# Optimization experiments

Hardware: AMD Instinct MI355X
Metric: run time of the kernel (lower is better)

Reference implementation:

```python
import jax, jax.numpy as jnp
import numpy as np

B, L, H = 16, 512, 1024
K_START, K_END = 5, 5
LN_EPS = 1e-12
NEG = 1e30


def _layer_norm(x, gamma, beta):
    mu = jnp.mean(x, axis=-1, keepdims=True)
    var = jnp.mean(jnp.square(x - mu), axis=-1, keepdims=True)
    return (x - mu) * jax.lax.rsqrt(var + LN_EPS) * gamma + beta


def setup_inputs() -> dict:
    key = jax.random.key(0)
    ks = jax.random.split(key, 10)
    s = 0.02
    sequence_data = jax.random.normal(ks[0], (B, L, H), jnp.float32)
    class_index = jax.random.randint(ks[1], (B,), 0, L, dtype=jnp.int32)
    paragraph_mask = (jax.random.uniform(ks[2], (B, L)) > 0.1).astype(jnp.float32)
    paragraph_mask = paragraph_mask.at[:, 0].set(1.0)  # guarantee >=1 valid position per row
    return {
        'sequence_data': sequence_data,
        'class_index': class_index,
        'paragraph_mask': paragraph_mask,
        'W_start': jax.random.normal(ks[3], (H, 1), jnp.float32) * s,
        'b_start': jnp.zeros((1,), jnp.float32),
        'W_end_in': jax.random.normal(ks[4], (2 * H, H), jnp.float32) * s,
        'b_end_in': jnp.zeros((H,), jnp.float32),
        'ln_gamma': jnp.ones((H,), jnp.float32),
        'ln_beta': jnp.zeros((H,), jnp.float32),
        'W_end_out': jax.random.normal(ks[5], (H, 1), jnp.float32) * s,
        'b_end_out': jnp.zeros((1,), jnp.float32),
        'W_ans_in': jax.random.normal(ks[6], (2 * H, H), jnp.float32) * s,
        'b_ans_in': jnp.zeros((H,), jnp.float32),
        'W_ans_out': jax.random.normal(ks[7], (H, 1), jnp.float32) * s,
    }


def reference(sequence_data, class_index, paragraph_mask,
              W_start, b_start, W_end_in, b_end_in, ln_gamma, ln_beta,
              W_end_out, b_end_out, W_ans_in, b_ans_in, W_ans_out):
    mask = paragraph_mask  # [b, l] float, 1 = valid

    # ---- start logits ----
    start_logits = jnp.einsum('blh,ho->bl', sequence_data, W_start) + b_start[0]  # [b,l]
    masked_start_logits = start_logits * mask - NEG * (1.0 - mask)
    start_predictions = jax.nn.log_softmax(masked_start_logits, axis=-1)

    # ---- beam search over start positions (inference branch) ----
    start_top_predictions, start_top_index = jax.lax.top_k(start_predictions, K_START)  # [b,k]
    # one-hot einsum gather 'blh,bkl->bkh' expressed as direct indexing
    start_features = jnp.take_along_axis(sequence_data, start_top_index[:, :, None], axis=1)  # [b,k,h]

    # end_logits inner dense on concat([tiled seq, tiled start_features]) along h:
    # split the [2h, h] kernel and broadcast-add instead of materializing the tiled concat.
    W1, W2 = W_end_in[:H], W_end_in[H:]
    inner = jnp.tanh(
        jnp.einsum('blh,hd->bld', sequence_data, W1)[:, :, None, :]
        + jnp.einsum('bkh,hd->bkd', start_features, W2)[:, None, :, :]
        + b_end_in
    )  # [b,l,k,h]
    inner = _layer_norm(inner, ln_gamma, ln_beta)
    end_logits = jnp.einsum('blkh,ho->blk', inner, W_end_out) + b_end_out[0]  # [b,l,k]
    end_logits = jnp.transpose(end_logits, (0, 2, 1))  # [b,k,l]

    mask_k = mask[:, None, :]  # [b,1,l]
    masked_end_logits = end_logits * mask_k - NEG * (1.0 - mask_k)
    end_predictions = jax.nn.log_softmax(masked_end_logits, axis=-1)

    end_top_predictions, _end_top_index = jax.lax.top_k(end_predictions, K_END)  # [b,k,k2]
    end_top_predictions = end_top_predictions.reshape(-1, K_START * K_END)

    # ---- answer (class) logits ----
    class_feature = sequence_data[jnp.arange(sequence_data.shape[0]), class_index]  # [b,h]
    start_p = jax.nn.softmax(masked_start_logits, axis=-1)
    start_feature = jnp.einsum('blh,bl->bh', sequence_data, start_p)
    answer_feature = jnp.concatenate([start_feature, class_feature], axis=-1)  # [b,2h]
    answer_feature = jnp.tanh(answer_feature @ W_ans_in + b_ans_in)  # dropout is identity at inference
    class_logits = (answer_feature @ W_ans_out)[:, 0]  # [b]

    return (start_predictions, end_predictions, masked_start_logits, masked_end_logits,
            start_top_predictions, end_top_predictions, class_logits)
```

## Files before the change

### kernel.cpp

```cpp
#include <hip/hip_runtime.h>
#include <math.h>

#define HD   1024
#define LSEQ 512
#define NB   16
#define KTOP 5
#define NEGV 1e30f

typedef __bf16 bf16x8 __attribute__((ext_vector_type(8)));
typedef float  f32x4  __attribute__((ext_vector_type(4)));

__device__ inline unsigned short f2bf(float f) {
  unsigned u = __float_as_uint(f);
  unsigned r = (u + 0x7FFFu + ((u >> 16) & 1u)) >> 16;
  return (unsigned short)r;
}
__device__ inline float bf2f(unsigned short u) {
  return __uint_as_float(((unsigned)u) << 16);
}

__device__ inline float fast_tanh(float x) {
  float e = __expf(-2.f * fabsf(x));
  float v = (1.f - e) / (1.f + e);
  return copysignf(v, x);
}

__device__ inline float tanh_scaled(float xs) {
  float e = __builtin_amdgcn_exp2f(xs);
  float r = __builtin_amdgcn_rcpf(1.f + e);
  return fmaf(-2.f, r, 1.f);
}

#define GLDS(g, l) __builtin_amdgcn_global_load_lds(                      \
    (const __attribute__((address_space(1))) unsigned int*)(g),          \
    (__attribute__((address_space(3))) unsigned int*)(l), 16, 0, 0)


__device__ __forceinline__ void sm_body(int row, const float* __restrict__ xin,
                                        float* __restrict__ lsm_out,
                                        float* __restrict__ top_out,
                                        float* __restrict__ p_out,
                                        int* __restrict__ idx_out) {
  __shared__ float redf[4];
  __shared__ int redi[4];
  __shared__ float bc_m, bc_s;
  __shared__ int bc_i;
  int t = threadIdx.x, lane = t & 63, wid = t >> 6;
  const float* x = xin + (size_t)row * LSEQ;
  float x0 = x[t], x1 = x[t + 256];

  float m = fmaxf(x0, x1);
#pragma unroll
  for (int off = 32; off; off >>= 1) m = fmaxf(m, __shfl_xor(m, off));
  if (lane == 0) redf[wid] = m;
  __syncthreads();
  if (t == 0) bc_m = fmaxf(fmaxf(redf[0], redf[1]), fmaxf(redf[2], redf[3]));
  __syncthreads();
  m = bc_m;

  float e0 = expf(x0 - m), e1 = expf(x1 - m);
  float s = e0 + e1;
#pragma unroll
  for (int off = 32; off; off >>= 1) s += __shfl_xor(s, off);
  if (lane == 0) redf[wid] = s;
  __syncthreads();
  if (t == 0) bc_s = redf[0] + redf[1] + redf[2] + redf[3];
  __syncthreads();
  s = bc_s;
  float ls = logf(s);

  lsm_out[(size_t)row * LSEQ + t] = x0 - m - ls;
  lsm_out[(size_t)row * LSEQ + t + 256] = x1 - m - ls;
  if (p_out) {
    float inv = 1.f / s;
    p_out[(size_t)row * LSEQ + t] = e0 * inv;
    p_out[(size_t)row * LSEQ + t + 256] = e1 * inv;
  }

  bool a0 = true, a1 = true;
  for (int it = 0; it < KTOP; ++it) {
    float v0 = a0 ? x0 : -INFINITY;
    float v1 = a1 ? x1 : -INFINITY;
    float bv = v0; int bi = t;
    if (v1 > bv) { bv = v1; bi = t + 256; }
#pragma unroll
    for (int off = 32; off; off >>= 1) {
      float ov = __shfl_xor(bv, off);
      int oi = __shfl_xor(bi, off);
      if (ov > bv || (ov == bv && oi < bi)) { bv = ov; bi = oi; }
    }
    __syncthreads();
    if (lane == 0) { redf[wid] = bv; redi[wid] = bi; }
    __syncthreads();
    if (t == 0) {
      float wv = redf[0]; int wi = redi[0];
      for (int w = 1; w < 4; ++w)
        if (redf[w] > wv || (redf[w] == wv && redi[w] < wi)) { wv = redf[w]; wi = redi[w]; }
      top_out[row * KTOP + it] = wv - m - ls;
      if (idx_out) idx_out[row * KTOP + it] = wi;
      bc_i = wi;
    }
    __syncthreads();
    int wi = bc_i;
    if (wi == t) a0 = false;
    if (wi == t + 256) a1 = false;
  }
}

__device__ __forceinline__ void gemm_body(int R0, int C0,
                                          const unsigned short* __restrict__ Abf,
                                          const unsigned short* __restrict__ Bt,
                                          unsigned short* __restrict__ X1) {
  __shared__ unsigned short SH[16384];
  unsigned short* As = SH;
  unsigned short* Bs = SH + 8192;
  int t = threadIdx.x;
  int w = t >> 6, lane = t & 63, ln = lane & 15, hi = lane >> 4;
  int wr = w >> 1, wc = w & 1;

  f32x4 acc[4][4] = {};

#define STAGE(kc)                                                             \
  do {                                                                        \
    _Pragma("unroll")                                                         \
    for (int p_ = 0; p_ < 4; ++p_) {                                          \
      int rr_ = p_ * 32 + (t >> 3);                                           \
      int cc_ = (t & 7) ^ (rr_ & 7);                                          \
      GLDS(Abf + (size_t)(R0 + rr_) * HD + (kc) + cc_ * 8,                    \
           As + p_ * 2048 + w * 512);                                         \
      GLDS(Bt + (size_t)(C0 + rr_) * HD + (kc) + cc_ * 8,                     \
           Bs + p_ * 2048 + w * 512);                                         \
    }                                                                         \
  } while (0)

  for (int it = 0; it < 16; ++it) {
    if (it) __syncthreads();
    STAGE(it * 64);
    asm volatile("s_waitcnt vmcnt(0)" ::: "memory");
    __builtin_amdgcn_s_barrier();
#pragma unroll
    for (int ks = 0; ks < 2; ++ks) {
      bf16x8 av[4], bv[4];
#pragma unroll
      for (int m = 0; m < 4; ++m) {
        int r = wr * 64 + m * 16 + ln;
        av[m] = *(const bf16x8*)(const void*)&As[r * 64 + (((ks * 4 + hi) ^ (r & 7)) * 8)];
      }
#pragma unroll
      for (int n = 0; n < 4; ++n) {
        int r = wc * 64 + n * 16 + ln;
        bv[n] = *(const bf16x8*)(const void*)&Bs[r * 64 + (((ks * 4 + hi) ^ (r & 7)) * 8)];
      }
#pragma unroll
      for (int m = 0; m < 4; ++m)
#pragma unroll
        for (int n = 0; n < 4; ++n)
          acc[m][n] = __builtin_amdgcn_mfma_f32_16x16x32_bf16(av[m], bv[n], acc[m][n], 0, 0, 0);
    }
  }
#undef STAGE

#pragma unroll
  for (int m = 0; m < 4; ++m)
#pragma unroll
    for (int j = 0; j < 4; ++j) {
      int row = R0 + wr * 64 + m * 16 + hi * 4 + j;
#pragma unroll
      for (int n = 0; n < 4; ++n) {
        int col = C0 + wc * 64 + n * 16 + ln;
        X1[(size_t)row * HD + col] = f2bf(acc[m][n][j]);
      }
    }
}

__device__ __forceinline__ void x2gemm_body(int cid,
                                            const unsigned short* __restrict__ seqb,
                                            const unsigned short* __restrict__ w2t,
                                            const int* __restrict__ idx,
                                            const float* __restrict__ bei,
                                            float* __restrict__ x2p) {
  __shared__ unsigned short SH2[16384];
  unsigned short* As = SH2;
  unsigned short* Bs = SH2 + 8192;
  int t = threadIdx.x;
  int w = t >> 6, lane = t & 63, ln = lane & 15, hi = lane >> 4;
  int wr = w >> 1, wc = w & 1;
  int C0 = cid * 128;

  size_t abase[4];
#pragma unroll
  for (int p_ = 0; p_ < 4; ++p_) {
    int rr = p_ * 32 + (t >> 3);
    int bk = rr < 80 ? rr : 0;
    int l = idx[bk];
    abase[p_] = ((size_t)((bk / KTOP) * LSEQ + l)) * HD;
  }

  f32x4 acc[4][4] = {};

#define STAGE2(kc)                                                            \
  do {                                                                        \
    _Pragma("unroll")                                                         \
    for (int p_ = 0; p_ < 4; ++p_) {                                          \
      int rr_ = p_ * 32 + (t >> 3);                                           \
      int cc_ = (t & 7) ^ (rr_ & 7);                                          \
      GLDS(seqb + abase[p_] + (kc) + cc_ * 8,                                 \
           As + p_ * 2048 + w * 512);                                         \
      GLDS(w2t + (size_t)(C0 + rr_) * HD + (kc) + cc_ * 8,                    \
           Bs + p_ * 2048 + w * 512);                                         \
    }                                                                         \
  } while (0)

  for (int it = 0; it < 16; ++it) {
    if (it) __syncthreads();
    STAGE2(it * 64);
    asm volatile("s_waitcnt vmcnt(0)" ::: "memory");
    __builtin_amdgcn_s_barrier();
#pragma unroll
    for (int ks = 0; ks < 2; ++ks) {
      bf16x8 av[4], bv[4];
#pragma unroll
      for (int m = 0; m < 4; ++m) {
        int r = wr * 64 + m * 16 + ln;
        av[m] = *(const bf16x8*)(const void*)&As[r * 64 + (((ks * 4 + hi) ^ (r & 7)) * 8)];
      }
#pragma unroll
      for (int n = 0; n < 4; ++n) {
        int r = wc * 64 + n * 16 + ln;
        bv[n] = *(const bf16x8*)(const void*)&Bs[r * 64 + (((ks * 4 + hi) ^ (r & 7)) * 8)];
      }
#pragma unroll
      for (int m = 0; m < 4; ++m)
#pragma unroll
        for (int n = 0; n < 4; ++n)
          acc[m][n] = __builtin_amdgcn_mfma_f32_16x16x32_bf16(av[m], bv[n], acc[m][n], 0, 0, 0);
    }
  }
#undef STAGE2

#pragma unroll
  for (int m = 0; m < 4; ++m)
#pragma unroll
    for (int j = 0; j < 4; ++j) {
      int row = wr * 64 + m * 16 + hi * 4 + j;
      if (row < 80) {
#pragma unroll
        for (int n = 0; n < 4; ++n) {
          int col = C0 + wc * 64 + n * 16 + ln;
          x2p[(size_t)row * HD + col] = acc[m][n][j] + bei[col];
        }
      }
    }
}

__device__ __forceinline__ void ansin_body(int q, const float* __restrict__ seq,
                                           const float* __restrict__ p_ws,
                                           const int* __restrict__ cls,
                                           float* __restrict__ pa,
                                           float* __restrict__ cf) {
  __shared__ float ps[16];
  int b = q >> 5, s = q & 31, t = threadIdx.x;
  if (t < 16) ps[t] = p_ws[b * LSEQ + s * 16 + t];
  __syncthreads();
  const float* sb = seq + (size_t)(b * LSEQ + s * 16) * HD;
  float4 acc = make_float4(0.f, 0.f, 0.f, 0.f);
#pragma unroll
  for (int r = 0; r < 16; ++r) {
    float4 v = *(const float4*)(sb + (size_t)r * HD + 4 * t);
    float p = ps[r];
    acc.x = fmaf(p, v.x, acc.x);
    acc.y = fmaf(p, v.y, acc.y);
    acc.z = fmaf(p, v.z, acc.z);
    acc.w = fmaf(p, v.w, acc.w);
  }
  *(float4*)(pa + ((size_t)b * 32 + s) * HD + 4 * t) = acc;
  if (s == 0) {
    int ci = cls[b];
    *(float4*)(cf + (size_t)b * HD + 4 * t) =
        *(const float4*)(seq + (size_t)(b * LSEQ + ci) * HD + 4 * t);
  }
}

__device__ __forceinline__ void endrow_body(int bx, const unsigned short* __restrict__ X1,
                                            const float* __restrict__ x2p,
                                            const float* __restrict__ gw_ws,
                                            const float* __restrict__ sgb_ws,
                                            const float* __restrict__ mask,
                                            float* __restrict__ mel) {
  __shared__ float x2s[KTOP * HD];
  const float A = 2.885390081777927f;
  int t = threadIdx.x, wave = t >> 6, lane = t & 63;
  int row = bx * 4 + wave;
  int b = row >> 9, l = row & 511;

  {
    const float4* src = (const float4*)(x2p + (size_t)b * KTOP * HD);
    float4* dst = (float4*)x2s;
    for (int i = t; i < KTOP * HD / 4; i += 256) {
      float4 v = src[i];
      dst[i] = make_float4(v.x * A, v.y * A, v.z * A, v.w * A);
    }
  }

  float xs[16], gwr[16];
  const unsigned short* xrow = X1 + (size_t)row * HD + lane * 4;
#pragma unroll
  for (int q = 0; q < 4; ++q) {
    ushort4 u = *(const ushort4*)(xrow + q * 256);
    xs[4 * q + 0] = bf2f(u.x) * A;
    xs[4 * q + 1] = bf2f(u.y) * A;
    xs[4 * q + 2] = bf2f(u.z) * A;
    xs[4 * q + 3] = bf2f(u.w) * A;
    float4 g = *(const float4*)(gw_ws + q * 256 + lane * 4);
    gwr[4 * q + 0] = g.x; gwr[4 * q + 1] = g.y;
    gwr[4 * q + 2] = g.z; gwr[4 * q + 3] = g.w;
  }
  float mv = mask[row];
  float sG = sgb_ws[0], sBW = sgb_ws[1];
  __syncthreads();

#pragma unroll
  for (int k = 0; k < KTOP; ++k) {
    float sv = 0.f, s2 = 0.f, sg = 0.f;
#pragma unroll
    for (int q = 0; q < 4; ++q) {
      float4 xq = *(const float4*)&x2s[k * HD + q * 256 + lane * 4];
      float v0 = tanh_scaled(xs[4 * q + 0] + xq.x);
      float v1 = tanh_scaled(xs[4 * q + 1] + xq.y);
      float v2 = tanh_scaled(xs[4 * q + 2] + xq.z);
      float v3 = tanh_scaled(xs[4 * q + 3] + xq.w);
      sv += v0 + v1 + v2 + v3;
      s2 = fmaf(v0, v0, s2); s2 = fmaf(v1, v1, s2);
      s2 = fmaf(v2, v2, s2); s2 = fmaf(v3, v3, s2);
      sg = fmaf(v0, gwr[4 * q + 0], sg); sg = fmaf(v1, gwr[4 * q + 1], sg);
      sg = fmaf(v2, gwr[4 * q + 2], sg); sg = fmaf(v3, gwr[4 * q + 3], sg);
    }
#pragma unroll
    for (int off = 32; off; off >>= 1) {
      sv += __shfl_xor(sv, off);
      s2 += __shfl_xor(s2, off);
      sg += __shfl_xor(sg, off);
    }
    if (lane == 0) {
      float mu = sv * (1.f / (float)HD);
      float var = s2 * (1.f / (float)HD) - mu * mu;
      float rr = rsqrtf(var + 1e-12f);
      float logit = rr * (sg - mu * sG) + sBW;
      mel[((size_t)b * KTOP + k) * LSEQ + l] = logit * mv - NEGV * (1.f - mv);
    }
  }
}

__device__ __forceinline__ void ansmid_body(int q, const float* __restrict__ pa,
                                            const float* __restrict__ cf,
                                            const float* __restrict__ Wai,
                                            float* __restrict__ pans) {
  __shared__ float a_s[128];
  int b = q >> 4, c = q & 15, t = threadIdx.x;
  if (t < 128) {
    int i = c * 128 + t;
    float av;
    if (i < HD) {
      av = 0.f;
#pragma unroll
      for (int s = 0; s < 32; ++s) av += pa[((size_t)b * 32 + s) * HD + i];
    } else {
      av = cf[(size_t)b * HD + (i - HD)];
    }
    a_s[t] = av;
  }
  __syncthreads();
  float4 acc = make_float4(0.f, 0.f, 0.f, 0.f);
#pragma unroll 8
  for (int r = 0; r < 128; ++r) {
    float4 wv = *(const float4*)(Wai + (size_t)(c * 128 + r) * HD + 4 * t);
    float a = a_s[r];
    acc.x = fmaf(a, wv.x, acc.x);
    acc.y = fmaf(a, wv.y, acc.y);
    acc.z = fmaf(a, wv.z, acc.z);
    acc.w = fmaf(a, wv.w, acc.w);
  }
  *(float4*)(pans + ((size_t)b * 16 + c) * HD + 4 * t) = acc;
}

__device__ __forceinline__ void ansfinal_body(int b, const float* __restrict__ pans,
                                              const float* __restrict__ bai,
                                              const float* __restrict__ Wao,
                                              float* __restrict__ out6) {
  __shared__ float red[4];
  int t = threadIdx.x, lane = t & 63, wid = t >> 6;
  float4 a = *(const float4*)(bai + 4 * t);
#pragma unroll
  for (int c = 0; c < 16; ++c) {
    float4 p = *(const float4*)(pans + ((size_t)b * 16 + c) * HD + 4 * t);
    a.x += p.x; a.y += p.y; a.z += p.z; a.w += p.w;
  }
  float4 wo = *(const float4*)(Wao + 4 * t);
  float part = fast_tanh(a.x) * wo.x + fast_tanh(a.y) * wo.y +
               fast_tanh(a.z) * wo.z + fast_tanh(a.w) * wo.w;
#pragma unroll
  for (int off = 32; off; off >>= 1) part += __shfl_xor(part, off);
  if (lane == 0) red[wid] = part;
  __syncthreads();
  if (t == 0) out6[b] = red[0] + red[1] + red[2] + red[3];
}


__global__ void k_prep(const float* __restrict__ seq,
                       unsigned short* __restrict__ seqb,
                       const float* __restrict__ Wst,
                       const float* __restrict__ bst,
                       const float* __restrict__ mask,
                       float* __restrict__ msl,
                       const float* __restrict__ Wei,
                       unsigned short* __restrict__ w1t,
                       unsigned short* __restrict__ w2t,
                       const float* __restrict__ gam,
                       const float* __restrict__ bet,
                       const float* __restrict__ Weo,
                       const float* __restrict__ beo,
                       float* __restrict__ gw_ws,
                       float* __restrict__ sgb_ws) {
  __shared__ unsigned short tile[32][33];
  __shared__ float redp[4][2];
  int bx = blockIdx.x;
  if (bx < 2048) {
    int wave = threadIdx.x >> 6, lane = threadIdx.x & 63;
    int row = bx * 4 + wave;
    const float4* s4 = (const float4*)(seq + (size_t)row * HD);
    const float4* w4 = (const float4*)Wst;
    ushort4* o4 = (ushort4*)(seqb + (size_t)row * HD);
    float acc = 0.f;
#pragma unroll
    for (int m = 0; m < 4; ++m) {
      int i = lane + 64 * m;
      float4 a = s4[i], w = w4[i];
      acc += a.x * w.x + a.y * w.y + a.z * w.z + a.w * w.w;
      ushort4 o;
      o.x = f2bf(a.x); o.y = f2bf(a.y); o.z = f2bf(a.z); o.w = f2bf(a.w);
      o4[i] = o;
    }
#pragma unroll
    for (int off = 32; off; off >>= 1) acc += __shfl_xor(acc, off);
    if (lane == 0) {
      float logit = acc + bst[0];
      float mv = mask[row];
      msl[row] = logit * mv - NEGV * (1.f - mv);
    }
  } else if (bx < 4096) {
    int tb = bx - 2048;
    const float* Wsrc = Wei + (tb >= 1024 ? (size_t)HD * HD : 0);
    unsigned short* Wdst = (tb >= 1024) ? w2t : w1t;
    int tb2 = tb & 1023;
    int h0 = (tb2 & 31) * 32, d0 = (tb2 >> 5) * 32;
    int tx = threadIdx.x & 31, ty = threadIdx.x >> 5;
#pragma unroll
    for (int i = 0; i < 4; ++i)
      tile[ty + 8 * i][tx] = f2bf(Wsrc[(size_t)(h0 + ty + 8 * i) * HD + d0 + tx]);
    __syncthreads();
#pragma unroll
    for (int i = 0; i < 4; ++i)
      Wdst[(size_t)(d0 + ty + 8 * i) * HD + h0 + tx] = tile[tx][ty + 8 * i];
  } else {
    int t = threadIdx.x, wave = t >> 6, lane = t & 63;
    float4 g = ((const float4*)gam)[t];
    float4 w = ((const float4*)Weo)[t];
    float4 bv = ((const float4*)bet)[t];
    float4 gwv = make_float4(g.x * w.x, g.y * w.y, g.z * w.z, g.w * w.w);
    ((float4*)gw_ws)[t] = gwv;
    float pg = gwv.x + gwv.y + gwv.z + gwv.w;
    float pb = bv.x * w.x + bv.y * w.y + bv.z * w.z + bv.w * w.w;
#pragma unroll
    for (int off = 32; off; off >>= 1) {
      pg += __shfl_xor(pg, off);
      pb += __shfl_xor(pb, off);
    }
    if (lane == 0) { redp[wave][0] = pg; redp[wave][1] = pb; }
    __syncthreads();
    if (t == 0) {
      sgb_ws[0] = redp[0][0] + redp[1][0] + redp[2][0] + redp[3][0];
      sgb_ws[1] = redp[0][1] + redp[1][1] + redp[2][1] + redp[3][1] + beo[0];
    }
  }
}

__global__ void k_softmax_topk(const float* __restrict__ xin,
                               float* __restrict__ lsm_out,
                               float* __restrict__ top_out,
                               float* __restrict__ p_out,
                               int* __restrict__ idx_out) {
  sm_body(blockIdx.x, xin, lsm_out, top_out, p_out, idx_out);
}

__launch_bounds__(256, 4)
__global__ void k_gsm(const unsigned short* __restrict__ Abf,
                      const unsigned short* __restrict__ Bt,
                      unsigned short* __restrict__ X1,
                      const float* __restrict__ msl,
                      float* __restrict__ lsm_out,
                      float* __restrict__ top_out,
                      float* __restrict__ p_out,
                      int* __restrict__ idx_out) {
  int id = blockIdx.x;
  if (id < 16) {
    sm_body(id, msl, lsm_out, top_out, p_out, idx_out);
  } else {
    int gid = id - 16;
    gemm_body((gid & 63) * 128, (gid >> 6) * 128, Abf, Bt, X1);
  }
}

__launch_bounds__(256, 4)
__global__ void k_x2a(const unsigned short* __restrict__ seqb,
                      const unsigned short* __restrict__ w2t,
                      const int* __restrict__ idx,
                      const float* __restrict__ bei,
                      float* __restrict__ x2p,
                      const float* __restrict__ seq,
                      const float* __restrict__ p_ws,
                      const int* __restrict__ cls,
                      float* __restrict__ pa,
                      float* __restrict__ cf) {
  int id = blockIdx.x;
  if (id < 8) x2gemm_body(id, seqb, w2t, idx, bei, x2p);
  else ansin_body(id - 8, seq, p_ws, cls, pa, cf);
}

__global__ void k_end2(const unsigned short* __restrict__ X1,
                       const float* __restrict__ x2p,
                       const float* __restrict__ gw_ws,
                       const float* __restrict__ sgb_ws,
                       const float* __restrict__ mask,
                       float* __restrict__ mel,
                       const float* __restrict__ pa,
                       const float* __restrict__ cf,
                       const float* __restrict__ Wai,
                       float* __restrict__ pans) {
  int bx = blockIdx.x;
  if (bx < 2048) endrow_body(bx, X1, x2p, gw_ws, sgb_ws, mask, mel);
  else ansmid_body(bx - 2048, pa, cf, Wai, pans);
}

__global__ void k_fin(const float* __restrict__ mel,
                      float* __restrict__ lsm_out,
                      float* __restrict__ top_out,
                      const float* __restrict__ pans,
                      const float* __restrict__ bai,
                      const float* __restrict__ Wao,
                      float* __restrict__ out6) {
  int bx = blockIdx.x;
  if (bx < NB * KTOP) sm_body(bx, mel, lsm_out, top_out, nullptr, nullptr);
  else ansfinal_body(bx - NB * KTOP, pans, bai, Wao, out6);
}

__global__ void k_x2init(const float* __restrict__ bei, float* __restrict__ x2p) {
  ((float4*)(x2p + (size_t)blockIdx.x * HD))[threadIdx.x] = ((const float4*)bei)[threadIdx.x];
}

__global__ void k_x2f(const float* __restrict__ seq, const int* __restrict__ idx,
                      const float* __restrict__ Wei, float* __restrict__ x2p) {
  __shared__ float srow[128];
  int q = blockIdx.x;
  int bk = q >> 3, s = q & 7, t = threadIdx.x;
  int b = bk / KTOP;
  int l = idx[bk];
  if (t < 128) srow[t] = seq[((size_t)(b * LSEQ + l)) * HD + s * 128 + t];
  __syncthreads();
  const float* W2 = Wei + (size_t)HD * HD + (size_t)s * 128 * HD;
  float4 acc = make_float4(0.f, 0.f, 0.f, 0.f);
#pragma unroll 8
  for (int h = 0; h < 128; ++h) {
    float4 wv = *(const float4*)(W2 + (size_t)h * HD + 4 * t);
    float sv = srow[h];
    acc.x = fmaf(sv, wv.x, acc.x);
    acc.y = fmaf(sv, wv.y, acc.y);
    acc.z = fmaf(sv, wv.z, acc.z);
    acc.w = fmaf(sv, wv.w, acc.w);
  }
  float* dst = x2p + (size_t)bk * HD + 4 * t;
  atomicAdd(dst + 0, acc.x);
  atomicAdd(dst + 1, acc.y);
  atomicAdd(dst + 2, acc.z);
  atomicAdd(dst + 3, acc.w);
}

__global__ void k_ansin_f(const float* __restrict__ seq, const float* __restrict__ p_ws,
                          const int* __restrict__ cls, float* __restrict__ pa,
                          float* __restrict__ cf) {
  ansin_body(blockIdx.x, seq, p_ws, cls, pa, cf);
}
__global__ void k_ansmid_f(const float* __restrict__ pa, const float* __restrict__ cf,
                           const float* __restrict__ Wai, float* __restrict__ pans) {
  ansmid_body(blockIdx.x, pa, cf, Wai, pans);
}

__launch_bounds__(256, 2)
__global__ void k_gemm_end_at(const unsigned short* __restrict__ Abf,
                              const unsigned short* __restrict__ Bt,
                              const float* __restrict__ x2p,
                              const float* __restrict__ gamma,
                              const float* __restrict__ Wout,
                              float* __restrict__ outp) {
  __shared__ unsigned short As[2][128 * 64];
  __shared__ unsigned short Bs[2][128 * 64];
  int t = threadIdx.x;
  int w = t >> 6, lane = t & 63, ln = lane & 15, hi = lane >> 4;
  int wr = w >> 1, wc = w & 1;
  int R0 = blockIdx.x * 128, C0 = blockIdx.y * 128;
  int b = R0 >> 9;
  f32x4 acc[4][4] = {};
#define STAGE(buf, kc)                                                        \
  do {                                                                        \
    _Pragma("unroll")                                                         \
    for (int p_ = 0; p_ < 4; ++p_) {                                          \
      int rr_ = p_ * 32 + (t >> 3);                                           \
      int cc_ = (t & 7) ^ (rr_ & 7);                                          \
      GLDS(Abf + (size_t)(R0 + rr_) * HD + (kc) + cc_ * 8,                    \
           &As[buf][p_ * 2048 + w * 512]);                                    \
      GLDS(Bt + (size_t)(C0 + rr_) * HD + (kc) + cc_ * 8,                     \
           &Bs[buf][p_ * 2048 + w * 512]);                                    \
    }                                                                         \
  } while (0)
  STAGE(0, 0);
  for (int it = 0; it < 16; ++it) {
    int cur = it & 1;
    if (it < 15) {
      STAGE(cur ^ 1, (it + 1) * 64);
      asm volatile("s_waitcnt vmcnt(8)" ::: "memory");
    } else {
      asm volatile("s_waitcnt vmcnt(0)" ::: "memory");
    }
    __builtin_amdgcn_s_barrier();
    __builtin_amdgcn_sched_barrier(0);
#pragma unroll
    for (int ks = 0; ks < 2; ++ks) {
      bf16x8 av[4], bv[4];
#pragma unroll
      for (int m = 0; m < 4; ++m) {
        int r = wr * 64 + m * 16 + ln;
        av[m] = *(const bf16x8*)(const void*)&As[cur][r * 64 + (((ks * 4 + hi) ^ (r & 7)) * 8)];
      }
#pragma unroll
      for (int n = 0; n < 4; ++n) {
        int r = wc * 64 + n * 16 + ln;
        bv[n] = *(const bf16x8*)(const void*)&Bs[cur][r * 64 + (((ks * 4 + hi) ^ (r & 7)) * 8)];
      }
#pragma unroll
      for (int m = 0; m < 4; ++m)
#pragma unroll
        for (int n = 0; n < 4; ++n)
          acc[m][n] = __builtin_amdgcn_mfma_f32_16x16x32_bf16(av[m], bv[n], acc[m][n], 0, 0, 0);
    }
    __builtin_amdgcn_sched_barrier(0);
    __builtin_amdgcn_s_barrier();
  }
#undef STAGE
  float gsv[4];
  float x2v[4][KTOP];
#pragma unroll
  for (int n = 0; n < 4; ++n) {
    int c = C0 + wc * 64 + n * 16 + ln;
    gsv[n] = gamma[c] * Wout[c];
#pragma unroll
    for (int k = 0; k < KTOP; ++k) x2v[n][k] = x2p[((size_t)b * KTOP + k) * HD + c];
  }
#pragma unroll
  for (int m = 0; m < 4; ++m)
#pragma unroll
    for (int j = 0; j < 4; ++j) {
      int row = R0 + wr * 64 + m * 16 + hi * 4 + j;
#pragma unroll
      for (int k = 0; k < KTOP; ++k) {
        float sv = 0.f, s2 = 0.f, sg = 0.f;
#pragma unroll
        for (int n = 0; n < 4; ++n) {
          float v = fast_tanh(acc[m][n][j] + x2v[n][k]);
          sv += v; s2 += v * v; sg += v * gsv[n];
        }
#pragma unroll
        for (int off = 8; off; off >>= 1) {
          sv += __shfl_xor(sv, off);
          s2 += __shfl_xor(s2, off);
          sg += __shfl_xor(sg, off);
        }
        if (ln == 0) {
          float* p = outp + ((size_t)row * KTOP + k) * 3;
          atomicAdd(p, sv);
          atomicAdd(p + 1, s2);
          atomicAdd(p + 2, sg);
        }
      }
    }
}

__global__ void k_end_final(const float* __restrict__ sums,
                            const float* __restrict__ gamma,
                            const float* __restrict__ beta,
                            const float* __restrict__ Wout,
                            const float* __restrict__ beo,
                            const float* __restrict__ mask,
                            float* __restrict__ mel) {
  int bk = blockIdx.x, b = bk / KTOP, k = bk % KTOP;
  int t = threadIdx.x, lane = t & 63, wid = t >> 6;
  __shared__ float red[4][2];
  float pg = 0.f, pb = 0.f;
  for (int i = t; i < HD; i += 256) {
    float wv = Wout[i];
    pg += gamma[i] * wv;
    pb += beta[i] * wv;
  }
#pragma unroll
  for (int off = 32; off; off >>= 1) {
    pg += __shfl_xor(pg, off);
    pb += __shfl_xor(pb, off);
  }
  if (lane == 0) { red[wid][0] = pg; red[wid][1] = pb; }
  __syncthreads();
  float sG = red[0][0] + red[1][0] + red[2][0] + red[3][0];
  float sBW = red[0][1] + red[1][1] + red[2][1] + red[3][1] + beo[0];
  for (int l = t; l < LSEQ; l += 256) {
    int row = b * LSEQ + l;
    const float* s = sums + ((size_t)row * KTOP + k) * 3;
    float sv = s[0], s2 = s[1], sg = s[2];
    float mu = sv * (1.f / (float)HD);
    float var = s2 * (1.f / (float)HD) - mu * mu;
    float rr = rsqrtf(var + 1e-12f);
    float logit = rr * (sg - mu * sG) + sBW;
    float mv = mask[row];
    mel[((size_t)b * KTOP + k) * LSEQ + l] = logit * mv - NEGV * (1.f - mv);
  }
}

extern "C" void kernel_launch(void* const* d_in, const int* in_sizes, int n_in,
                              void* d_out, int out_size, void* d_ws, size_t ws_size,
                              hipStream_t stream) {
  (void)in_sizes; (void)n_in; (void)out_size;
  const float* seq = (const float*)d_in[0];
  const int*   cls = (const int*)d_in[1];
  const float* mask = (const float*)d_in[2];
  const float* Wst = (const float*)d_in[3];
  const float* bst = (const float*)d_in[4];
  const float* Wei = (const float*)d_in[5];
  const float* bei = (const float*)d_in[6];
  const float* gam = (const float*)d_in[7];
  const float* bet = (const float*)d_in[8];
  const float* Weo = (const float*)d_in[9];
  const float* beo = (const float*)d_in[10];
  const float* Wai = (const float*)d_in[11];
  const float* bai = (const float*)d_in[12];
  const float* Wao = (const float*)d_in[13];

  float* out = (float*)d_out;
  float* out0 = out;
  float* out1 = out0 + 8192;
  float* out2 = out1 + 40960;
  float* out3 = out2 + 8192;
  float* out4 = out3 + 40960;
  float* out5 = out4 + 80;
  float* out6 = out5 + 400;

  char* p = (char*)d_ws;
  unsigned short* seqb = (unsigned short*)p;  p += (size_t)8192 * 1024 * 2;
  unsigned short* w1t  = (unsigned short*)p;  p += (size_t)1024 * 1024 * 2;
  unsigned short* w2t  = (unsigned short*)p;  p += (size_t)1024 * 1024 * 2;
  float* p_ws   = (float*)p;                  p += 8192 * 4;
  int*   idx_ws = (int*)p;                    p += 128 * 4;
  float* x2p    = (float*)p;                  p += (size_t)80 * 1024 * 4;
  float* gw_ws  = (float*)p;                  p += 1024 * 4;
  float* sgb_ws = (float*)p;                  p += 4 * 4;
  float* pa     = (float*)p;                  p += (size_t)16 * 32 * 1024 * 4;
  float* cf     = (float*)p;                  p += (size_t)16 * 1024 * 4;
  float* pans   = (float*)p;                  p += (size_t)16 * 16 * 1024 * 4;
  unsigned short* x1 = (unsigned short*)p;
  float* sums = (float*)p;
  size_t base = (size_t)(p - (char*)d_ws);
  size_t need_big = base + (size_t)8192 * 1024 * 2;
  size_t need_small = base + (size_t)8192 * KTOP * 3 * 4;

  k_prep<<<4097, 256, 0, stream>>>(seq, seqb, Wst, bst, mask, out2, Wei, w1t, w2t,
                                   gam, bet, Weo, beo, gw_ws, sgb_ws);

  if (ws_size >= need_big) {
    k_gsm<<<528, 256, 0, stream>>>(seqb, w1t, x1, out2, out0, out4, p_ws, idx_ws);
    k_x2a<<<520, 256, 0, stream>>>(seqb, w2t, idx_ws, bei, x2p,
                                   seq, p_ws, cls, pa, cf);
    k_end2<<<2304, 256, 0, stream>>>(x1, x2p, gw_ws, sgb_ws, mask, out3,
                                     pa, cf, Wai, pans);
  } else if (ws_size >= need_small) {
    k_softmax_topk<<<NB, 256, 0, stream>>>(out2, out0, out4, p_ws, idx_ws);
    k_x2init<<<80, 256, 0, stream>>>(bei, x2p);
    k_x2f<<<640, 256, 0, stream>>>(seq, idx_ws, Wei, x2p);
    hipMemsetAsync(sums, 0, (size_t)8192 * KTOP * 3 * sizeof(float), stream);
    k_gemm_end_at<<<dim3(64, 8), 256, 0, stream>>>(seqb, w1t, x2p, gam, Weo, sums);
    k_end_final<<<NB * KTOP, 256, 0, stream>>>(sums, gam, bet, Weo, beo, mask, out3);
    k_ansin_f<<<512, 256, 0, stream>>>(seq, p_ws, cls, pa, cf);
    k_ansmid_f<<<256, 256, 0, stream>>>(pa, cf, Wai, pans);
  }

  k_fin<<<96, 256, 0, stream>>>(out3, out1, out5, pans, bai, Wao, out6);
}
```

Measured before the change: 87.92 us.

## Rebalance fused kernels: move answer pooling into GEMM launch, ansmid into x2 launch

The start-softmax-weighted pooling now recomputes the softmax probabilities per block and reads bf16 sequence data. This lets it run in the first fused launch, interleaved with the big GEMM tiles. The answer-mid matvec moves into the x2 GEMM launch, leaving the end-row kernel to do only its own work. Shared memory is shared across the fused bodies through explicit pointers. The aim is to shorten the critical path by overlapping the small answer-branch work with the heavy GEMM phases. The cost is redundant softmax work per block and bf16 precision for the pooled feature.

```diff
diff --git a/kernel.cpp b/kernel.cpp
--- a/kernel.cpp
+++ b/kernel.cpp
@@ -36,15 +36,15 @@
     (__attribute__((address_space(3))) unsigned int*)(l), 16, 0, 0)
 
 
-__device__ __forceinline__ void sm_body(int row, const float* __restrict__ xin,
+__device__ __forceinline__ void sm_body(float* sc, int row, const float* __restrict__ xin,
                                         float* __restrict__ lsm_out,
                                         float* __restrict__ top_out,
                                         float* __restrict__ p_out,
                                         int* __restrict__ idx_out) {
-  __shared__ float redf[4];
-  __shared__ int redi[4];
-  __shared__ float bc_m, bc_s;
-  __shared__ int bc_i;
+  float* redf = sc;
+  int* redi = (int*)(sc + 4);
+  float* bc = sc + 8;
+  int* bci = (int*)(sc + 10);
   int t = threadIdx.x, lane = t & 63, wid = t >> 6;
   const float* x = xin + (size_t)row * LSEQ;
   float x0 = x[t], x1 = x[t + 256];
@@ -54,9 +54,9 @@
   for (int off = 32; off; off >>= 1) m = fmaxf(m, __shfl_xor(m, off));
   if (lane == 0) redf[wid] = m;
   __syncthreads();
-  if (t == 0) bc_m = fmaxf(fmaxf(redf[0], redf[1]), fmaxf(redf[2], redf[3]));
-  __syncthreads();
-  m = bc_m;
+  if (t == 0) bc[0] = fmaxf(fmaxf(redf[0], redf[1]), fmaxf(redf[2], redf[3]));
+  __syncthreads();
+  m = bc[0];
 
   float e0 = expf(x0 - m), e1 = expf(x1 - m);
   float s = e0 + e1;
@@ -64,9 +64,9 @@
   for (int off = 32; off; off >>= 1) s += __shfl_xor(s, off);
   if (lane == 0) redf[wid] = s;
   __syncthreads();
-  if (t == 0) bc_s = redf[0] + redf[1] + redf[2] + redf[3];
-  __syncthreads();
-  s = bc_s;
+  if (t == 0) bc[1] = redf[0] + redf[1] + redf[2] + redf[3];
+  __syncthreads();
+  s = bc[1];
   float ls = logf(s);
 
   lsm_out[(size_t)row * LSEQ + t] = x0 - m - ls;
@@ -98,20 +98,19 @@
         if (redf[w] > wv || (redf[w] == wv && redi[w] < wi)) { wv = redf[w]; wi = redi[w]; }
       top_out[row * KTOP + it] = wv - m - ls;
       if (idx_out) idx_out[row * KTOP + it] = wi;
-      bc_i = wi;
+      bci[0] = wi;
     }
     __syncthreads();
-    int wi = bc_i;
+    int wi = bci[0];
     if (wi == t) a0 = false;
     if (wi == t + 256) a1 = false;
   }
 }
 
-__device__ __forceinline__ void gemm_body(int R0, int C0,
+__device__ __forceinline__ void gemm_body(unsigned short* SH, int R0, int C0,
                                           const unsigned short* __restrict__ Abf,
                                           const unsigned short* __restrict__ Bt,
                                           unsigned short* __restrict__ X1) {
-  __shared__ unsigned short SH[16384];
   unsigned short* As = SH;
   unsigned short* Bs = SH + 8192;
   int t = threadIdx.x;
@@ -173,13 +172,12 @@
     }
 }
 
-__device__ __forceinline__ void x2gemm_body(int cid,
+__device__ __forceinline__ void x2gemm_body(unsigned short* SH2, int cid,
                                             const unsigned short* __restrict__ seqb,
                                             const unsigned short* __restrict__ w2t,
                                             const int* __restrict__ idx,
                                             const float* __restrict__ bei,
                                             float* __restrict__ x2p) {
-  __shared__ unsigned short SH2[16384];
   unsigned short* As = SH2;
   unsigned short* Bs = SH2 + 8192;
   int t = threadIdx.x;
@@ -253,6 +251,59 @@
     }
 }
 
+__device__ __forceinline__ void ansin_ms_body(float* sc, int q,
+                                              const unsigned short* __restrict__ seqb,
+                                              const float* __restrict__ seq,
+                                              const float* __restrict__ msl,
+                                              const int* __restrict__ cls,
+                                              float* __restrict__ pa,
+                                              float* __restrict__ cf) {
+  float* ared = sc;
+  float* abc = sc + 4;
+  float* ps = sc + 6;
+  int b = q >> 5, sl = q & 31, t = threadIdx.x;
+  int lane = t & 63, wid = t >> 6;
+
+  const float* x = msl + (size_t)b * LSEQ;
+  float x0 = x[t], x1 = x[t + 256];
+  float m = fmaxf(x0, x1);
+#pragma unroll
+  for (int off = 32; off; off >>= 1) m = fmaxf(m, __shfl_xor(m, off));
+  if (lane == 0) ared[wid] = m;
+  __syncthreads();
+  if (t == 0) abc[0] = fmaxf(fmaxf(ared[0], ared[1]), fmaxf(ared[2], ared[3]));
+  __syncthreads();
+  m = abc[0];
+  float e = expf(x0 - m) + expf(x1 - m);
+#pragma unroll
+  for (int off = 32; off; off >>= 1) e += __shfl_xor(e, off);
+  if (lane == 0) ared[wid] = e;
+  __syncthreads();
+  if (t == 0) abc[1] = ared[0] + ared[1] + ared[2] + ared[3];
+  __syncthreads();
+  float inv = 1.f / abc[1];
+  if (t < 16) ps[t] = expf(x[sl * 16 + t] - m) * inv;
+  __syncthreads();
+
+  const unsigned short* sb = seqb + (size_t)(b * LSEQ + sl * 16) * HD;
+  float4 acc = make_float4(0.f, 0.f, 0.f, 0.f);
+#pragma unroll
+  for (int r = 0; r < 16; ++r) {
+    ushort4 u = *(const ushort4*)(sb + (size_t)r * HD + 4 * t);
+    float p = ps[r];
+    acc.x = fmaf(p, bf2f(u.x), acc.x);
+    acc.y = fmaf(p, bf2f(u.y), acc.y);
+    acc.z = fmaf(p, bf2f(u.z), acc.z);
+    acc.w = fmaf(p, bf2f(u.w), acc.w);
+  }
+  *(float4*)(pa + ((size_t)b * 32 + sl) * HD + 4 * t) = acc;
+  if (sl == 0) {
+    int ci = cls[b];
+    *(float4*)(cf + (size_t)b * HD + 4 * t) =
+        *(const float4*)(seq + (size_t)(b * LSEQ + ci) * HD + 4 * t);
+  }
+}
+
 __device__ __forceinline__ void ansin_body(int q, const float* __restrict__ seq,
                                            const float* __restrict__ p_ws,
                                            const int* __restrict__ cls,
@@ -351,11 +402,10 @@
   }
 }
 
-__device__ __forceinline__ void ansmid_body(int q, const float* __restrict__ pa,
+__device__ __forceinline__ void ansmid_body(float* a_s, int q, const float* __restrict__ pa,
                                             const float* __restrict__ cf,
                                             const float* __restrict__ Wai,
                                             float* __restrict__ pans) {
-  __shared__ float a_s[128];
   int b = q >> 4, c = q & 15, t = threadIdx.x;
   if (t < 128) {
     int i = c * 128 + t;
@@ -383,11 +433,10 @@
   *(float4*)(pans + ((size_t)b * 16 + c) * HD + 4 * t) = acc;
 }
 
-__device__ __forceinline__ void ansfinal_body(int b, const float* __restrict__ pans,
+__device__ __forceinline__ void ansfinal_body(float* red, int b, const float* __restrict__ pans,
                                               const float* __restrict__ bai,
                                               const float* __restrict__ Wao,
                                               float* __restrict__ out6) {
-  __shared__ float red[4];
   int t = threadIdx.x, lane = t & 63, wid = t >> 6;
   float4 a = *(const float4*)(bai + 4 * t);
 #pragma unroll
@@ -489,7 +538,8 @@
                                float* __restrict__ top_out,
                                float* __restrict__ p_out,
                                int* __restrict__ idx_out) {
-  sm_body(blockIdx.x, xin, lsm_out, top_out, p_out, idx_out);
+  __shared__ float sc[32];
+  sm_body(sc, blockIdx.x, xin, lsm_out, top_out, p_out, idx_out);
 }
 
 __launch_bounds__(256, 4)
@@ -499,31 +549,39 @@
                       const float* __restrict__ msl,
                       float* __restrict__ lsm_out,
                       float* __restrict__ top_out,
-                      float* __restrict__ p_out,
-                      int* __restrict__ idx_out) {
+                      int* __restrict__ idx_out,
+                      const unsigned short* __restrict__ seqb,
+                      const float* __restrict__ seq,
+                      const int* __restrict__ cls,
+                      float* __restrict__ pa,
+                      float* __restrict__ cf) {
+  __shared__ unsigned short SH[16384];
   int id = blockIdx.x;
-  if (id < 16) {
-    sm_body(id, msl, lsm_out, top_out, p_out, idx_out);
+  int grp = id >> 4, j = id & 15;
+  if (j < 8) {
+    int g = grp * 8 + j;
+    if (g < 512) gemm_body(SH, (g & 63) * 128, (g >> 6) * 128, Abf, Bt, X1);
   } else {
-    int gid = id - 16;
-    gemm_body((gid & 63) * 128, (gid >> 6) * 128, Abf, Bt, X1);
+    int o = grp * 8 + (j - 8);
+    if (o < 16) sm_body((float*)SH, o, msl, lsm_out, top_out, nullptr, idx_out);
+    else if (o < 528) ansin_ms_body((float*)SH, o - 16, seqb, seq, msl, cls, pa, cf);
   }
 }
 
 __launch_bounds__(256, 4)
-__global__ void k_x2a(const unsigned short* __restrict__ seqb,
+__global__ void k_x2g(const unsigned short* __restrict__ seqb,
                       const unsigned short* __restrict__ w2t,
                       const int* __restrict__ idx,
                       const float* __restrict__ bei,
                       float* __restrict__ x2p,
-                      const float* __restrict__ seq,
-                      const float* __restrict__ p_ws,
-                      const int* __restrict__ cls,
-                      float* __restrict__ pa,
-                      float* __restrict__ cf) {
+                      const float* __restrict__ pa,
+                      const float* __restrict__ cf,
+                      const float* __restrict__ Wai,
+                      float* __restrict__ pans) {
+  __shared__ unsigned short SH2[16384];
   int id = blockIdx.x;
-  if (id < 8) x2gemm_body(id, seqb, w2t, idx, bei, x2p);
-  else ansin_body(id - 8, seq, p_ws, cls, pa, cf);
+  if (id < 8) x2gemm_body(SH2, id, seqb, w2t, idx, bei, x2p);
+  else ansmid_body((float*)SH2, id - 8, pa, cf, Wai, pans);
 }
 
 __global__ void k_end2(const unsigned short* __restrict__ X1,
@@ -531,14 +589,8 @@
                        const float* __restrict__ gw_ws,
                        const float* __restrict__ sgb_ws,
                        const float* __restrict__ mask,
-                       float* __restrict__ mel,
-                       const float* __restrict__ pa,
-                       const float* __restrict__ cf,
-                       const float* __restrict__ Wai,
-                       float* __restrict__ pans) {
-  int bx = blockIdx.x;
-  if (bx < 2048) endrow_body(bx, X1, x2p, gw_ws, sgb_ws, mask, mel);
-  else ansmid_body(bx - 2048, pa, cf, Wai, pans);
+                       float* __restrict__ mel) {
+  endrow_body(blockIdx.x, X1, x2p, gw_ws, sgb_ws, mask, mel);
 }
 
 __global__ void k_fin(const float* __restrict__ mel,
@@ -548,9 +600,10 @@
                       const float* __restrict__ bai,
                       const float* __restrict__ Wao,
                       float* __restrict__ out6) {
+  __shared__ float sc[32];
   int bx = blockIdx.x;
-  if (bx < NB * KTOP) sm_body(bx, mel, lsm_out, top_out, nullptr, nullptr);
-  else ansfinal_body(bx - NB * KTOP, pans, bai, Wao, out6);
+  if (bx < NB * KTOP) sm_body(sc, bx, mel, lsm_out, top_out, nullptr, nullptr);
+  else ansfinal_body(sc, bx - NB * KTOP, pans, bai, Wao, out6);
 }
 
 __global__ void k_x2init(const float* __restrict__ bei, float* __restrict__ x2p) {
@@ -591,7 +644,8 @@
 }
 __global__ void k_ansmid_f(const float* __restrict__ pa, const float* __restrict__ cf,
                            const float* __restrict__ Wai, float* __restrict__ pans) {
-  ansmid_body(blockIdx.x, pa, cf, Wai, pans);
+  __shared__ float a_s[128];
+  ansmid_body(a_s, blockIdx.x, pa, cf, Wai, pans);
 }
 
 __launch_bounds__(256, 2)
@@ -781,11 +835,10 @@
                                    gam, bet, Weo, beo, gw_ws, sgb_ws);
 
   if (ws_size >= need_big) {
-    k_gsm<<<528, 256, 0, stream>>>(seqb, w1t, x1, out2, out0, out4, p_ws, idx_ws);
-    k_x2a<<<520, 256, 0, stream>>>(seqb, w2t, idx_ws, bei, x2p,
-                                   seq, p_ws, cls, pa, cf);
-    k_end2<<<2304, 256, 0, stream>>>(x1, x2p, gw_ws, sgb_ws, mask, out3,
-                                     pa, cf, Wai, pans);
+    k_gsm<<<1056, 256, 0, stream>>>(seqb, w1t, x1, out2, out0, out4, idx_ws,
+                                    seqb, seq, cls, pa, cf);
+    k_x2g<<<264, 256, 0, stream>>>(seqb, w2t, idx_ws, bei, x2p, pa, cf, Wai, pans);
+    k_end2<<<2048, 256, 0, stream>>>(x1, x2p, gw_ws, sgb_ws, mask, out3);
   } else if (ws_size >= need_small) {
     k_softmax_topk<<<NB, 256, 0, stream>>>(out2, out0, out4, p_ws, idx_ws);
     k_x2init<<<80, 256, 0, stream>>>(bei, x2p);
```

After: 93.24 us. +6.1%, slower.

## Factor tanh exponentials and process 16 rows per block with DPP reductions

Applied to the files above, without the earlier changes.

The end-logit row kernel now precomputes exp2 of the scaled x2 beam features once per block in shared memory and exp2 of each x1 element once. The tanh of the sum becomes 1 - 2/(1 + e1*e2), which removes one exp per (row, k, h) element. Each wave now handles four rows with 16 lanes per row, reducing through DPP row shuffles instead of a full-wave shfl_xor tree, and the grid drops from 2048 to 512 end-row blocks. The risk is overflow or inf from the product of exponentials at large arguments, plus fewer blocks for latency hiding.

```diff
diff --git a/kernel.cpp b/kernel.cpp
--- a/kernel.cpp
+++ b/kernel.cpp
@@ -25,10 +25,17 @@
   return copysignf(v, x);
 }
 
-__device__ inline float tanh_scaled(float xs) {
-  float e = __builtin_amdgcn_exp2f(xs);
-  float r = __builtin_amdgcn_rcpf(1.f + e);
-  return fmaf(-2.f, r, 1.f);
+__device__ inline float dpp_row_reduce16(float v) {
+  int t;
+  t = __builtin_amdgcn_update_dpp(0, __float_as_int(v), 0x128, 0xf, 0xf, true);
+  v += __int_as_float(t);
+  t = __builtin_amdgcn_update_dpp(0, __float_as_int(v), 0x124, 0xf, 0xf, true);
+  v += __int_as_float(t);
+  t = __builtin_amdgcn_update_dpp(0, __float_as_int(v), 0x122, 0xf, 0xf, true);
+  v += __int_as_float(t);
+  t = __builtin_amdgcn_update_dpp(0, __float_as_int(v), 0x121, 0xf, 0xf, true);
+  v += __int_as_float(t);
+  return v;
 }
 
 #define GLDS(g, l) __builtin_amdgcn_global_load_lds(                      \
@@ -287,61 +294,53 @@
                                             const float* __restrict__ sgb_ws,
                                             const float* __restrict__ mask,
                                             float* __restrict__ mel) {
-  __shared__ float x2s[KTOP * HD];
+  __shared__ float x2e[KTOP * HD];
   const float A = 2.885390081777927f;
   int t = threadIdx.x, wave = t >> 6, lane = t & 63;
-  int row = bx * 4 + wave;
+  int g = lane >> 4, l16 = lane & 15;
+  int row = bx * 16 + wave * 4 + g;
   int b = row >> 9, l = row & 511;
 
   {
-    const float4* src = (const float4*)(x2p + (size_t)b * KTOP * HD);
-    float4* dst = (float4*)x2s;
-    for (int i = t; i < KTOP * HD / 4; i += 256) {
-      float4 v = src[i];
-      dst[i] = make_float4(v.x * A, v.y * A, v.z * A, v.w * A);
-    }
-  }
-
-  float xs[16], gwr[16];
-  const unsigned short* xrow = X1 + (size_t)row * HD + lane * 4;
-#pragma unroll
-  for (int q = 0; q < 4; ++q) {
-    ushort4 u = *(const ushort4*)(xrow + q * 256);
-    xs[4 * q + 0] = bf2f(u.x) * A;
-    xs[4 * q + 1] = bf2f(u.y) * A;
-    xs[4 * q + 2] = bf2f(u.z) * A;
-    xs[4 * q + 3] = bf2f(u.w) * A;
-    float4 g = *(const float4*)(gw_ws + q * 256 + lane * 4);
-    gwr[4 * q + 0] = g.x; gwr[4 * q + 1] = g.y;
-    gwr[4 * q + 2] = g.z; gwr[4 * q + 3] = g.w;
+    const float* src = x2p + (size_t)b * KTOP * HD;
+    for (int i = t; i < KTOP * HD; i += 256)
+      x2e[i] = __builtin_amdgcn_exp2f(src[i] * A);
   }
   float mv = mask[row];
   float sG = sgb_ws[0], sBW = sgb_ws[1];
   __syncthreads();
 
+  float av[KTOP] = {}, a2[KTOP] = {}, ag[KTOP] = {};
+  const unsigned short* xrow = X1 + (size_t)row * HD;
+#pragma unroll 4
+  for (int j = 0; j < 16; ++j) {
+    int col = j * 64 + l16 * 4;
+    ushort4 u = *(const ushort4*)(xrow + col);
+    float4 gwv = *(const float4*)(gw_ws + col);
+    float e0 = __builtin_amdgcn_exp2f(bf2f(u.x) * A);
+    float e1 = __builtin_amdgcn_exp2f(bf2f(u.y) * A);
+    float e2 = __builtin_amdgcn_exp2f(bf2f(u.z) * A);
+    float e3 = __builtin_amdgcn_exp2f(bf2f(u.w) * A);
+#pragma unroll
+    for (int k = 0; k < KTOP; ++k) {
+      float4 xq = *(const float4*)&x2e[k * HD + col];
+      float v0 = fmaf(-2.f, __builtin_amdgcn_rcpf(fmaf(e0, xq.x, 1.f)), 1.f);
+      float v1 = fmaf(-2.f, __builtin_amdgcn_rcpf(fmaf(e1, xq.y, 1.f)), 1.f);
+      float v2 = fmaf(-2.f, __builtin_amdgcn_rcpf(fmaf(e2, xq.z, 1.f)), 1.f);
+      float v3 = fmaf(-2.f, __builtin_amdgcn_rcpf(fmaf(e3, xq.w, 1.f)), 1.f);
+      av[k] += v0 + v1 + v2 + v3;
+      a2[k] = fmaf(v0, v0, a2[k]); a2[k] = fmaf(v1, v1, a2[k]);
+      a2[k] = fmaf(v2, v2, a2[k]); a2[k] = fmaf(v3, v3, a2[k]);
+      ag[k] = fmaf(v0, gwv.x, ag[k]); ag[k] = fmaf(v1, gwv.y, ag[k]);
+      ag[k] = fmaf(v2, gwv.z, ag[k]); ag[k] = fmaf(v3, gwv.w, ag[k]);
+    }
+  }
 #pragma unroll
   for (int k = 0; k < KTOP; ++k) {
-    float sv = 0.f, s2 = 0.f, sg = 0.f;
-#pragma unroll
-    for (int q = 0; q < 4; ++q) {
-      float4 xq = *(const float4*)&x2s[k * HD + q * 256 + lane * 4];
-      float v0 = tanh_scaled(xs[4 * q + 0] + xq.x);
-      float v1 = tanh_scaled(xs[4 * q + 1] + xq.y);
-      float v2 = tanh_scaled(xs[4 * q + 2] + xq.z);
-      float v3 = tanh_scaled(xs[4 * q + 3] + xq.w);
-      sv += v0 + v1 + v2 + v3;
-      s2 = fmaf(v0, v0, s2); s2 = fmaf(v1, v1, s2);
-      s2 = fmaf(v2, v2, s2); s2 = fmaf(v3, v3, s2);
-      sg = fmaf(v0, gwr[4 * q + 0], sg); sg = fmaf(v1, gwr[4 * q + 1], sg);
-      sg = fmaf(v2, gwr[4 * q + 2], sg); sg = fmaf(v3, gwr[4 * q + 3], sg);
-    }
-#pragma unroll
-    for (int off = 32; off; off >>= 1) {
-      sv += __shfl_xor(sv, off);
-      s2 += __shfl_xor(s2, off);
-      sg += __shfl_xor(sg, off);
-    }
-    if (lane == 0) {
+    float sv = dpp_row_reduce16(av[k]);
+    float s2 = dpp_row_reduce16(a2[k]);
+    float sg = dpp_row_reduce16(ag[k]);
+    if (l16 == 0) {
       float mu = sv * (1.f / (float)HD);
       float var = s2 * (1.f / (float)HD) - mu * mu;
       float rr = rsqrtf(var + 1e-12f);
@@ -537,8 +536,8 @@
                        const float* __restrict__ Wai,
                        float* __restrict__ pans) {
   int bx = blockIdx.x;
-  if (bx < 2048) endrow_body(bx, X1, x2p, gw_ws, sgb_ws, mask, mel);
-  else ansmid_body(bx - 2048, pa, cf, Wai, pans);
+  if (bx < 512) endrow_body(bx, X1, x2p, gw_ws, sgb_ws, mask, mel);
+  else ansmid_body(bx - 512, pa, cf, Wai, pans);
 }
 
 __global__ void k_fin(const float* __restrict__ mel,
@@ -784,8 +783,8 @@
     k_gsm<<<528, 256, 0, stream>>>(seqb, w1t, x1, out2, out0, out4, p_ws, idx_ws);
     k_x2a<<<520, 256, 0, stream>>>(seqb, w2t, idx_ws, bei, x2p,
                                    seq, p_ws, cls, pa, cf);
-    k_end2<<<2304, 256, 0, stream>>>(x1, x2p, gw_ws, sgb_ws, mask, out3,
-                                     pa, cf, Wai, pans);
+    k_end2<<<768, 256, 0, stream>>>(x1, x2p, gw_ws, sgb_ws, mask, out3,
+                                    pa, cf, Wai, pans);
   } else if (ws_size >= need_small) {
     k_softmax_topk<<<NB, 256, 0, stream>>>(out2, out0, out4, p_ws, idx_ws);
     k_x2init<<<80, 256, 0, stream>>>(bei, x2p);
```

Result: no change. 86.78 us (-1.3%).
